# Optimization experiments

Measured on AMD Instinct MI355X. Metric: run time of the kernel, lower is better.

## Reference

```python
import jax, jax.numpy as jnp
import numpy as np

D_MODEL = 1024
NUM_HEADS = 16
D_HEAD = D_MODEL // NUM_HEADS
ROPE_THETA = 10000.0


def _rope(x, pos):
    # x: [..., S, d_head]; rotate consecutive pairs (2i, 2i+1)
    half = x.shape[-1] // 2
    inv_freq = ROPE_THETA ** (-jnp.arange(half, dtype=jnp.float32) * 2.0 / x.shape[-1])
    ang = pos[:, None].astype(jnp.float32) * inv_freq[None, :]  # [S, half]
    cos, sin = jnp.cos(ang), jnp.sin(ang)
    x1, x2 = x[..., 0::2], x[..., 1::2]
    r1 = x1 * cos - x2 * sin
    r2 = x1 * sin + x2 * cos
    return jnp.stack([r1, r2], axis=-1).reshape(x.shape)


def setup_inputs() -> dict:
    key = jax.random.key(0)
    ks = jax.random.split(key, 5)
    s = 1.0 / np.sqrt(D_MODEL)
    return {
        "q_weight": jax.random.normal(ks[0], (D_MODEL, D_MODEL), jnp.float32) * s,
        "k_weight": jax.random.normal(ks[1], (D_MODEL, D_MODEL), jnp.float32) * s,
        "v_weight": jax.random.normal(ks[2], (D_MODEL, D_MODEL), jnp.float32) * s,
        "o_weight": jax.random.normal(ks[3], (D_MODEL, D_MODEL), jnp.float32) * s,
        "in_features": jax.random.normal(ks[4], (2, 2048, D_MODEL), jnp.float32),
    }


def reference(q_weight, k_weight, v_weight, o_weight, in_features):
    S = in_features.shape[-2]
    qw = q_weight.reshape(NUM_HEADS, D_HEAD, D_MODEL)
    kw = k_weight.reshape(NUM_HEADS, D_HEAD, D_MODEL)
    vw = v_weight.reshape(NUM_HEADS, D_HEAD, D_MODEL)
    # [B, H, S, d_head]
    q = jnp.einsum('bsj,nhj->bnsh', in_features, qw)
    k = jnp.einsum('bsj,nhj->bnsh', in_features, kw)
    v = jnp.einsum('bsj,nhj->bnsh', in_features, vw)
    pos = jnp.arange(S)
    q = _rope(q, pos)
    k = _rope(k, pos)
    scale = 1.0 / jnp.sqrt(jnp.asarray(D_HEAD, dtype=q.dtype))
    scores = jnp.einsum('bnqh,bnkh->bnqk', q, k) * scale  # [B,H,S,S]
    causal = jnp.tril(jnp.ones((S, S), dtype=bool))
    scores = jnp.where(causal, scores, jnp.asarray(-jnp.inf, dtype=scores.dtype))
    attn = jax.nn.softmax(scores, axis=-1)
    out = jnp.einsum('bnqk,bnkh->bnqh', attn, v)  # [B,H,S,d_head]
    out = jnp.swapaxes(out, -2, -3).reshape(*out.shape[:-3], S, D_MODEL)
    return jnp.einsum('ji,bki->bkj', o_weight, out)
```

## Files before the change

### kernel.cpp

```cpp
#include <hip/hip_runtime.h>
#include <math.h>

typedef __attribute__((ext_vector_type(8))) short bf16x8;
typedef __attribute__((ext_vector_type(4))) short bf16x4;
typedef __attribute__((ext_vector_type(4))) float f32x4;
typedef __attribute__((ext_vector_type(2))) unsigned int u32x2;

static constexpr int D_MODEL = 1024;
static constexpr int SEQ = 2048;
static constexpr int BATCH = 2;
static constexpr int M_TOT = BATCH * SEQ;

__device__ __forceinline__ unsigned short f2bf(float f) {
  unsigned int u = __builtin_bit_cast(unsigned int, f);
  u += 0x7fffu + ((u >> 16) & 1u);
  return (unsigned short)(u >> 16);
}

__device__ __forceinline__ unsigned int cvtpk(float lo, float hi) {
  unsigned int r;
  asm volatile("v_cvt_pk_bf16_f32 %0, %1, %2" : "=v"(r) : "v"(lo), "v"(hi));
  return r;
}

__device__ __forceinline__ void gld16(const unsigned short* g, unsigned short* l) {
  __builtin_amdgcn_global_load_lds(
      (const __attribute__((address_space(1))) unsigned int*)g,
      (__attribute__((address_space(3))) unsigned int*)l, 16, 0, 0);
}

__global__ void prep_all(const float* __restrict__ x,
                         const float* __restrict__ qw, const float* __restrict__ kw,
                         const float* __restrict__ vw, const float* __restrict__ ow,
                         unsigned short* __restrict__ Xb,
                         unsigned short* __restrict__ Wqb,
                         float2* __restrict__ ct2) {
  constexpr int NX = M_TOT * D_MODEL / 4;
  constexpr int NW = D_MODEL * D_MODEL;
  const int i = blockIdx.x * blockDim.x + threadIdx.x;
  if (i < NX) {
    const float4 v = reinterpret_cast<const float4*>(x)[i];
    ushort4 o;
    o.x = f2bf(v.x); o.y = f2bf(v.y); o.z = f2bf(v.z); o.w = f2bf(v.w);
    reinterpret_cast<ushort4*>(Xb)[i] = o;
  } else if (i < NX + NW) {
    const int k = i - NX;
    const int which = k >> 18;
    const int off = k & 262143;
    const float* src = (which == 0) ? qw : (which == 1) ? kw : (which == 2) ? vw : ow;
    const float4 v = reinterpret_cast<const float4*>(src)[off];
    ushort4 o;
    o.x = f2bf(v.x); o.y = f2bf(v.y); o.z = f2bf(v.z); o.w = f2bf(v.w);
    reinterpret_cast<ushort4*>(Wqb)[k] = o;
  } else {
    const int k = i - NX - NW;
    const int s = k >> 5;
    const int p = k & 31;
    const float inv_freq = powf(10000.0f, -(float)p / 32.0f);
    const float ang = (float)s * inv_freq;
    const int psw = p ^ (((s >> 2) & 1) << 3);
    float2 cs; cs.x = cosf(ang); cs.y = sinf(ang);
    ct2[s * 32 + psw] = cs;
  }
}

template <int BM, int BN, int MODE>
__global__ __launch_bounds__(256, 2)
void gemm2(const unsigned short* __restrict__ A,
           const unsigned short* __restrict__ W,
           unsigned short* __restrict__ Qd,
           unsigned short* __restrict__ Kd,
           unsigned short* __restrict__ Vd,
           float* __restrict__ Fd,
           const float2* __restrict__ ct2) {
  constexpr int MI = BM / 32, NI = BN / 32;
  constexpr int NKT = D_MODEL / 64;
  constexpr int LOADS = BM / 32 + BN / 32;
  __shared__ __align__(16) unsigned short smem[2 * (BM + BN) * 64];
  unsigned short* Asm = smem;
  unsigned short* Bsm = smem + 2 * BM * 64;
  const int tid  = threadIdx.x;
  const int lane = tid & 63;
  const int wave = tid >> 6;
  const int wm = wave >> 1, wn = wave & 1;
  const int m0 = blockIdx.y * BM;
  const int n0 = blockIdx.x * BN;
  const int lr = lane & 15, lg = lane >> 4;

  auto stage = [&](int buf, int kt) {
    const int k0 = kt * 64;
#pragma unroll
    for (int c = 0; c < BM / 32; ++c) {
      const int ch = c * 4 + wave;
      const int row = ch * 8 + (lane >> 3);
      gld16(&A[(size_t)(m0 + row) * D_MODEL + k0 + ((lane & 7) ^ (row & 7)) * 8],
            &Asm[buf * BM * 64 + ch * 512]);
    }
#pragma unroll
    for (int c = 0; c < BN / 32; ++c) {
      const int ch = c * 4 + wave;
      const int row = ch * 8 + (lane >> 3);
      gld16(&W[(size_t)(n0 + row) * D_MODEL + k0 + ((lane & 7) ^ (row & 7)) * 8],
            &Bsm[buf * BN * 64 + ch * 512]);
    }
  };

  f32x4 acc[MI][NI] = {};

  stage(0, 0);
  stage(1, 1);
  __builtin_amdgcn_sched_barrier(0);

  for (int kt = 0; kt < NKT; ++kt) {
    const int cur = kt & 1;
    if (kt + 1 < NKT) {
      if constexpr (LOADS == 8) asm volatile("s_waitcnt vmcnt(8)" ::: "memory");
      else                      asm volatile("s_waitcnt vmcnt(6)" ::: "memory");
    } else {
      asm volatile("s_waitcnt vmcnt(0)" ::: "memory");
    }
    __builtin_amdgcn_s_barrier();
    __builtin_amdgcn_sched_barrier(0);

    bf16x8 af[MI][2], bfr[NI][2];
#pragma unroll
    for (int i = 0; i < MI; ++i)
#pragma unroll
      for (int ks = 0; ks < 2; ++ks) {
        const int R = wm * (BM / 2) + i * 16 + lr;
        const int p = (ks * 4 + lg) ^ (R & 7);
        af[i][ks] = *reinterpret_cast<const bf16x8*>(&Asm[cur * BM * 64 + R * 64 + p * 8]);
      }
#pragma unroll
    for (int j = 0; j < NI; ++j)
#pragma unroll
      for (int ks = 0; ks < 2; ++ks) {
        const int R = wn * (BN / 2) + j * 16 + lr;
        const int p = (ks * 4 + lg) ^ (R & 7);
        bfr[j][ks] = *reinterpret_cast<const bf16x8*>(&Bsm[cur * BN * 64 + R * 64 + p * 8]);
      }
    asm volatile("s_waitcnt lgkmcnt(0)" ::: "memory");
    __builtin_amdgcn_sched_barrier(0);
    __builtin_amdgcn_s_barrier();
    __builtin_amdgcn_sched_barrier(0);

    if (kt + 2 < NKT) stage(cur, kt + 2);
    __builtin_amdgcn_sched_barrier(0);

#pragma unroll
    for (int ks = 0; ks < 2; ++ks)
#pragma unroll
      for (int i = 0; i < MI; ++i)
#pragma unroll
        for (int j = 0; j < NI; ++j)
          acc[i][j] = __builtin_amdgcn_mfma_f32_16x16x32_bf16(af[i][ks], bfr[j][ks], acc[i][j], 0, 0, 0);
  }

  if constexpr (MODE == 2) {
#pragma unroll
    for (int i = 0; i < MI; ++i)
#pragma unroll
      for (int j = 0; j < NI; ++j)
#pragma unroll
        for (int r = 0; r < 4; ++r) {
          const int gm = m0 + wm * (BM / 2) + i * 16 + lg * 4 + r;
          const int gc = n0 + wn * (BN / 2) + j * 16 + lr;
          Fd[(size_t)gm * D_MODEL + gc] = acc[i][j][r];
        }
  } else {
    const int t = n0 >> 10;
    const int b = m0 >> 11;
    const int s_base = m0 & 2047;
    if (t < 2) {
      unsigned short* dstQ = (t == 0) ? Qd : Kd;
      const unsigned short* gsrc = (const unsigned short*)(ct2 + (size_t)s_base * 32);
#pragma unroll
      for (int it = 0; it < 8; ++it) {
        const int ch = wave * 8 + it;
        gld16(&gsrc[ch * 512 + lane * 8], &smem[ch * 512]);
      }
      asm volatile("s_waitcnt vmcnt(0)" ::: "memory");
      __builtin_amdgcn_sched_barrier(0);
      __builtin_amdgcn_s_barrier();
      const float2* tbl = (const float2*)smem;
      const int nbase = (n0 & 1023) >> 6;
#pragma unroll
      for (int i = 0; i < MI; ++i) {
#pragma unroll
        for (int j = 0; j < NI; ++j) {
#pragma unroll
          for (int r = 0; r < 4; ++r) {
            const int sl = wm * (BM / 2) + i * 16 + lg * 4 + r;
            const int h  = j * 16 + lr;
            const int psw = (h >> 1) ^ (((sl >> 2) & 1) << 3);
            const float2 cs = tbl[sl * 32 + psw];
            float x = acc[i][j][r];
            const float part = __shfl_xor(x, 1, 64);
            x = (h & 1) ? (part * cs.y + x * cs.x) : (x * cs.x - part * cs.y);
            const int n = nbase + wn;
            dstQ[(size_t)((b * 16 + n) * SEQ + s_base + sl) * 64 + h] = f2bf(x);
          }
        }
      }
    } else {
      unsigned short* tile = smem;
      const int row = tid >> 2;
      const int ck  = tid & 3;
      for (int pass = 0; pass < 2; ++pass) {
        __builtin_amdgcn_s_barrier();
        if (wn == pass) {
#pragma unroll
          for (int i = 0; i < MI; ++i)
#pragma unroll
            for (int j = 0; j < NI; ++j)
#pragma unroll
              for (int r = 0; r < 4; ++r)
                tile[(j * 16 + lr) * 136 + wm * 64 + i * 16 + lg * 4 + r] = f2bf(acc[i][j][r]);
        }
        asm volatile("s_waitcnt lgkmcnt(0)" ::: "memory");
        __builtin_amdgcn_sched_barrier(0);
        __builtin_amdgcn_s_barrier();
        const int c = (n0 & 1023) + pass * 64 + row;
        const int n = c >> 6, h = c & 63;
        unsigned short* vrow = &Vd[(size_t)((b * 16 + n) * 64 + h) * SEQ + s_base + ck * 32];
        const unsigned short* lrow = &tile[row * 136 + ck * 32];
#pragma unroll
        for (int k = 0; k < 4; ++k)
          *reinterpret_cast<bf16x8*>(&vrow[k * 8]) = *reinterpret_cast<const bf16x8*>(&lrow[k * 8]);
      }
    }
  }
}

__global__ __launch_bounds__(128, 2)
void attn_kernel(const unsigned short* __restrict__ Q,
                 const unsigned short* __restrict__ K,
                 const unsigned short* __restrict__ Vt,
                 unsigned short* __restrict__ AO) {
  __shared__ __align__(16) unsigned short Ksh[2][4096];
  __shared__ __align__(16) unsigned short Vsh[2][4096];
  const int bn   = blockIdx.x;
  const int y    = blockIdx.y;
  const int a    = y & 7, bsel = y >> 3;
  const int j    = (bsel == 0) ? (31 - a) : (bsel == 1) ? (16 + a)
                 : (bsel == 2) ? (15 - a) : a;
  const int wave = threadIdx.x >> 6;
  const int lane = threadIdx.x & 63;
  const int lr = lane & 15, lg = lane >> 4;
  const int q0 = j * 64 + wave * 32;
  const unsigned short* Qh = Q  + (size_t)bn * SEQ * 64;
  const unsigned short* Kh = K  + (size_t)bn * SEQ * 64;
  const unsigned short* Vh = Vt + (size_t)bn * 64 * SEQ;
  const int b = bn >> 4, n = bn & 15;

  const int srow8 = lane >> 3;
  const int scolb = ((lane & 7) ^ srow8) * 8;

  auto stage = [&](int buf, int k0) {
#pragma unroll
    for (int c = 0; c < 4; ++c) {
      const int ch = wave * 4 + c;
      const int row = ch * 8 + srow8;
      gld16(&Kh[(size_t)(k0 + row) * 64 + scolb], &Ksh[buf][ch * 512]);
      gld16(&Vh[(size_t)row * SEQ + k0 + scolb], &Vsh[buf][ch * 512]);
    }
  };

  constexpr float KL2E = 0.125f * 1.44269504088896f;
  const int nt = j + 1;

  bf16x8 qf[2][2];
#pragma unroll
  for (int mi = 0; mi < 2; ++mi)
#pragma unroll
    for (int ks = 0; ks < 2; ++ks)
      qf[mi][ks] = *reinterpret_cast<const bf16x8*>(
          &Qh[(size_t)(q0 + mi * 16 + lr) * 64 + ks * 32 + lg * 8]);
  asm volatile("s_waitcnt vmcnt(0)" ::: "memory");
  __builtin_amdgcn_sched_barrier(0);

  f32x4 o[2][4] = {};
  float ls[2] = {0.f, 0.f};

  stage(0, 0);
  stage(1, 64);
  __builtin_amdgcn_sched_barrier(0);

  for (int t = 0; t < nt; ++t) {
    const int cur = t & 1;
    const int k0 = t * 64;
    if (t + 1 < nt) { asm volatile("s_waitcnt vmcnt(8)" ::: "memory"); }
    else            { asm volatile("s_waitcnt vmcnt(0)" ::: "memory"); }
    __builtin_amdgcn_s_barrier();
    __builtin_amdgcn_sched_barrier(0);

    const unsigned short* Kc = &Ksh[cur][0];
    const unsigned short* Vc = &Vsh[cur][0];

    bf16x8 kf[4][2];
#pragma unroll
    for (int nj = 0; nj < 4; ++nj)
#pragma unroll
      for (int ks = 0; ks < 2; ++ks) {
        const int R = nj * 16 + lr;
        const int p = (ks * 4 + lg) ^ (R & 7);
        kf[nj][ks] = *reinterpret_cast<const bf16x8*>(&Kc[R * 64 + p * 8]);
      }
    f32x4 sf[2][4] = {};
    __builtin_amdgcn_s_setprio(1);
#pragma unroll
    for (int nj = 0; nj < 4; ++nj)
#pragma unroll
      for (int ks = 0; ks < 2; ++ks)
#pragma unroll
        for (int mi = 0; mi < 2; ++mi)
          sf[mi][nj] = __builtin_amdgcn_mfma_f32_16x16x32_bf16(kf[nj][ks], qf[mi][ks], sf[mi][nj], 0, 0, 0);
    __builtin_amdgcn_s_setprio(0);

    bf16x4 vB[4][4];
#pragma unroll
    for (int nj = 0; nj < 4; ++nj)
#pragma unroll
      for (int hf = 0; hf < 4; ++hf) {
        const int R = hf * 16 + lr;
        const int c = nj * 2 + (lg >> 1);
        const int p = ((c ^ (R & 7)) << 3) + (lg & 1) * 4;
        vB[nj][hf] = *reinterpret_cast<const bf16x4*>(&Vc[R * 64 + p]);
      }

    u32x2 w[2][4];
    if (k0 + 63 <= q0) {
#pragma unroll
      for (int mi = 0; mi < 2; ++mi)
#pragma unroll
        for (int nj = 0; nj < 4; ++nj) {
          const float p0 = __builtin_amdgcn_exp2f(sf[mi][nj][0] * KL2E);
          const float p1 = __builtin_amdgcn_exp2f(sf[mi][nj][1] * KL2E);
          const float p2 = __builtin_amdgcn_exp2f(sf[mi][nj][2] * KL2E);
          const float p3 = __builtin_amdgcn_exp2f(sf[mi][nj][3] * KL2E);
          ls[mi] += (p0 + p1) + (p2 + p3);
          w[mi][nj][0] = cvtpk(p0, p1);
          w[mi][nj][1] = cvtpk(p2, p3);
        }
    } else {
#pragma unroll
      for (int mi = 0; mi < 2; ++mi) {
        const int qrow = q0 + mi * 16 + lr;
#pragma unroll
        for (int nj = 0; nj < 4; ++nj) {
          const int kb = k0 + nj * 16 + lg * 4;
          float p[4];
#pragma unroll
          for (int r = 0; r < 4; ++r)
            p[r] = (kb + r <= qrow) ? __builtin_amdgcn_exp2f(sf[mi][nj][r] * KL2E) : 0.0f;
          ls[mi] += (p[0] + p[1]) + (p[2] + p[3]);
          w[mi][nj][0] = cvtpk(p[0], p[1]);
          w[mi][nj][1] = cvtpk(p[2], p[3]);
        }
      }
    }

    asm volatile("s_waitcnt lgkmcnt(0)" ::: "memory");
    __builtin_amdgcn_sched_barrier(0);
    __builtin_amdgcn_s_barrier();
    __builtin_amdgcn_sched_barrier(0);

    if (t + 2 < nt) stage(cur, (t + 2) * 64);
    __builtin_amdgcn_sched_barrier(0);

    __builtin_amdgcn_s_setprio(1);
#pragma unroll
    for (int nj = 0; nj < 4; ++nj)
#pragma unroll
      for (int hf = 0; hf < 4; ++hf)
#pragma unroll
        for (int mi = 0; mi < 2; ++mi)
          o[mi][hf] = __builtin_amdgcn_mfma_f32_16x16x16bf16_1k(
              __builtin_bit_cast(bf16x4, w[mi][nj]), vB[nj][hf], o[mi][hf], 0, 0, 0);
    __builtin_amdgcn_s_setprio(0);
  }

#pragma unroll
  for (int mi = 0; mi < 2; ++mi) {
    float s = ls[mi];
    s += __shfl_xor(s, 16, 64);
    s += __shfl_xor(s, 32, 64);
    ls[mi] = s;
  }
#pragma unroll
  for (int mi = 0; mi < 2; ++mi)
#pragma unroll
    for (int r = 0; r < 4; ++r) {
      const float sv = __shfl(ls[mi], lg * 4 + r, 64);
      const float inv = 1.0f / sv;
      const int srow = q0 + mi * 16 + lg * 4 + r;
#pragma unroll
      for (int hf = 0; hf < 4; ++hf) {
        const int h = hf * 16 + lr;
        AO[(size_t)(b * SEQ + srow) * D_MODEL + n * 64 + h] = f2bf(o[mi][hf][r] * inv);
      }
    }
}

extern "C" void kernel_launch(void* const* d_in, const int* in_sizes, int n_in,
                              void* d_out, int out_size, void* d_ws, size_t ws_size,
                              hipStream_t stream) {
  const float* qw = (const float*)d_in[0];
  const float* kw = (const float*)d_in[1];
  const float* vw = (const float*)d_in[2];
  const float* ow = (const float*)d_in[3];
  const float* x  = (const float*)d_in[4];

  char* ws = (char*)d_ws;
  const size_t XB = (size_t)M_TOT * D_MODEL * 2;
  const size_t WB = (size_t)D_MODEL * D_MODEL * 2;
  unsigned short* Xb  = (unsigned short*)ws;  ws += XB;
  unsigned short* Wqb = (unsigned short*)ws;  ws += WB;
  unsigned short* Wkb = (unsigned short*)ws;  ws += WB;
  unsigned short* Wvb = (unsigned short*)ws;  ws += WB;
  unsigned short* Wob = (unsigned short*)ws;  ws += WB;
  unsigned short* Qr  = (unsigned short*)ws;  ws += XB;
  unsigned short* Kr  = (unsigned short*)ws;  ws += XB;
  unsigned short* Vt  = (unsigned short*)ws;  ws += XB;
  unsigned short* AO  = (unsigned short*)ws;  ws += XB;
  float2* ct2 = (float2*)ws;  ws += (size_t)SEQ * 32 * 8;
  (void)Wkb; (void)Wvb;

  constexpr int PREP_ITEMS = M_TOT * D_MODEL / 4 + D_MODEL * D_MODEL + SEQ * 32;
  prep_all<<<(PREP_ITEMS + 255) / 256, 256, 0, stream>>>(x, qw, kw, vw, ow, Xb, Wqb, ct2);

  gemm2<128, 128, 0><<<dim3(3072 / 128, M_TOT / 128), 256, 0, stream>>>(
      Xb, Wqb, Qr, Kr, Vt, nullptr, ct2);

  attn_kernel<<<dim3(BATCH * 16, 32), 128, 0, stream>>>(Qr, Kr, Vt, AO);

  gemm2<128, 64, 2><<<dim3(D_MODEL / 64, M_TOT / 128), 256, 0, stream>>>(
      AO, Wob, nullptr, nullptr, nullptr, (float*)d_out, nullptr);
}
```

Measured before the change: 103.8 us.

## Enlarge attention query tiles and split long causal rows across two blocks

The attention kernel now uses 256 threads per block covering 128 query rows, so each K/V tile staged in shared memory is reused by four waves instead of two. For the eight longest query tiles, the key range is split into two halves handled by separate blocks. Each half writes unnormalized partial outputs and row sums into reused workspace buffers, and a new merge kernel adds the halves and normalizes. The intent is to balance causal work across blocks and improve K/V reuse. The cost is an extra kernel launch, bf16 rounding of the partial outputs, and extra global traffic.

```diff
diff --git a/kernel.cpp b/kernel.cpp
--- a/kernel.cpp
+++ b/kernel.cpp
@@ -15,6 +15,10 @@
   unsigned int u = __builtin_bit_cast(unsigned int, f);
   u += 0x7fffu + ((u >> 16) & 1u);
   return (unsigned short)(u >> 16);
+}
+
+__device__ __forceinline__ float bf2f(unsigned short u) {
+  return __builtin_bit_cast(float, (unsigned int)u << 16);
 }
 
 __device__ __forceinline__ unsigned int cvtpk(float lo, float hi) {
@@ -232,22 +236,26 @@
   }
 }
 
-__global__ __launch_bounds__(128, 2)
+__global__ __launch_bounds__(256, 2)
 void attn_kernel(const unsigned short* __restrict__ Q,
                  const unsigned short* __restrict__ K,
                  const unsigned short* __restrict__ Vt,
-                 unsigned short* __restrict__ AO) {
+                 unsigned short* __restrict__ AO,
+                 unsigned short* __restrict__ po,
+                 float* __restrict__ pl) {
   __shared__ __align__(16) unsigned short Ksh[2][4096];
   __shared__ __align__(16) unsigned short Vsh[2][4096];
   const int bn   = blockIdx.x;
   const int y    = blockIdx.y;
-  const int a    = y & 7, bsel = y >> 3;
-  const int j    = (bsel == 0) ? (31 - a) : (bsel == 1) ? (16 + a)
-                 : (bsel == 2) ? (15 - a) : a;
+  const bool split = (y < 16);
+  const int j    = split ? (15 - (y >> 1)) : (23 - y);
+  const int half = split ? (y & 1) : 0;
+  const int t0   = (split && half) ? (j + 1) : 0;
+  const int tend = (split && !half) ? (j + 1) : (2 * j + 2);
   const int wave = threadIdx.x >> 6;
   const int lane = threadIdx.x & 63;
   const int lr = lane & 15, lg = lane >> 4;
-  const int q0 = j * 64 + wave * 32;
+  const int q0 = j * 128 + wave * 32;
   const unsigned short* Qh = Q  + (size_t)bn * SEQ * 64;
   const unsigned short* Kh = K  + (size_t)bn * SEQ * 64;
   const unsigned short* Vh = Vt + (size_t)bn * 64 * SEQ;
@@ -258,8 +266,8 @@
 
   auto stage = [&](int buf, int k0) {
 #pragma unroll
-    for (int c = 0; c < 4; ++c) {
-      const int ch = wave * 4 + c;
+    for (int c = 0; c < 2; ++c) {
+      const int ch = wave * 2 + c;
       const int row = ch * 8 + srow8;
       gld16(&Kh[(size_t)(k0 + row) * 64 + scolb], &Ksh[buf][ch * 512]);
       gld16(&Vh[(size_t)row * SEQ + k0 + scolb], &Vsh[buf][ch * 512]);
@@ -267,7 +275,6 @@
   };
 
   constexpr float KL2E = 0.125f * 1.44269504088896f;
-  const int nt = j + 1;
 
   bf16x8 qf[2][2];
 #pragma unroll
@@ -282,15 +289,15 @@
   f32x4 o[2][4] = {};
   float ls[2] = {0.f, 0.f};
 
-  stage(0, 0);
-  stage(1, 64);
+  stage(0, t0 * 64);
+  stage(1, (t0 + 1) * 64);
   __builtin_amdgcn_sched_barrier(0);
 
-  for (int t = 0; t < nt; ++t) {
-    const int cur = t & 1;
+  for (int t = t0; t < tend; ++t) {
+    const int cur = (t - t0) & 1;
     const int k0 = t * 64;
-    if (t + 1 < nt) { asm volatile("s_waitcnt vmcnt(8)" ::: "memory"); }
-    else            { asm volatile("s_waitcnt vmcnt(0)" ::: "memory"); }
+    if (t + 1 < tend) { asm volatile("s_waitcnt vmcnt(4)" ::: "memory"); }
+    else              { asm volatile("s_waitcnt vmcnt(0)" ::: "memory"); }
     __builtin_amdgcn_s_barrier();
     __builtin_amdgcn_sched_barrier(0);
 
@@ -365,7 +372,7 @@
     __builtin_amdgcn_s_barrier();
     __builtin_amdgcn_sched_barrier(0);
 
-    if (t + 2 < nt) stage(cur, (t + 2) * 64);
+    if (t + 2 < tend) stage(cur, (t + 2) * 64);
     __builtin_amdgcn_sched_barrier(0);
 
     __builtin_amdgcn_s_setprio(1);
@@ -387,19 +394,62 @@
     s += __shfl_xor(s, 32, 64);
     ls[mi] = s;
   }
-#pragma unroll
-  for (int mi = 0; mi < 2; ++mi)
-#pragma unroll
-    for (int r = 0; r < 4; ++r) {
-      const float sv = __shfl(ls[mi], lg * 4 + r, 64);
-      const float inv = 1.0f / sv;
-      const int srow = q0 + mi * 16 + lg * 4 + r;
-#pragma unroll
-      for (int hf = 0; hf < 4; ++hf) {
-        const int h = hf * 16 + lr;
-        AO[(size_t)(b * SEQ + srow) * D_MODEL + n * 64 + h] = f2bf(o[mi][hf][r] * inv);
-      }
-    }
+
+  if (!split) {
+#pragma unroll
+    for (int mi = 0; mi < 2; ++mi)
+#pragma unroll
+      for (int r = 0; r < 4; ++r) {
+        const float sv = __shfl(ls[mi], lg * 4 + r, 64);
+        const float inv = 1.0f / sv;
+        const int srow = q0 + mi * 16 + lg * 4 + r;
+#pragma unroll
+        for (int hf = 0; hf < 4; ++hf) {
+          const int h = hf * 16 + lr;
+          AO[(size_t)(b * SEQ + srow) * D_MODEL + n * 64 + h] = f2bf(o[mi][hf][r] * inv);
+        }
+      }
+  } else {
+    const int pb = (bn * 8 + (j - 8)) * 2 + half;
+    unsigned short* pod = po + (size_t)pb * (128 * 64);
+    float* pld = pl + (size_t)pb * 128;
+    if (lg == 0) {
+#pragma unroll
+      for (int mi = 0; mi < 2; ++mi)
+        pld[wave * 32 + mi * 16 + lr] = ls[mi];
+    }
+#pragma unroll
+    for (int mi = 0; mi < 2; ++mi)
+#pragma unroll
+      for (int r = 0; r < 4; ++r) {
+        const int row = wave * 32 + mi * 16 + lg * 4 + r;
+#pragma unroll
+        for (int hf = 0; hf < 4; ++hf)
+          pod[row * 64 + hf * 16 + lr] = f2bf(o[mi][hf][r]);
+      }
+  }
+}
+
+__global__ void attn_merge(const unsigned short* __restrict__ po,
+                           const float* __restrict__ pl,
+                           unsigned short* __restrict__ AO) {
+  const int i = blockIdx.x * blockDim.x + threadIdx.x;
+  const int g   = i & 7;
+  const int row = (i >> 3) & 127;
+  const int jj  = (i >> 10) & 7;
+  const int bn  = i >> 13;
+  const int pb0 = (bn * 8 + jj) * 2;
+  const float l = pl[pb0 * 128 + row] + pl[(pb0 + 1) * 128 + row];
+  const float inv = 1.0f / l;
+  const bf16x8 a = *reinterpret_cast<const bf16x8*>(&po[(size_t)pb0 * 8192 + row * 64 + g * 8]);
+  const bf16x8 c = *reinterpret_cast<const bf16x8*>(&po[(size_t)(pb0 + 1) * 8192 + row * 64 + g * 8]);
+  bf16x8 out;
+#pragma unroll
+  for (int e = 0; e < 8; ++e)
+    out[e] = (short)f2bf((bf2f((unsigned short)a[e]) + bf2f((unsigned short)c[e])) * inv);
+  const int s = (jj + 8) * 128 + row;
+  const int b = bn >> 4, n = bn & 15;
+  *reinterpret_cast<bf16x8*>(&AO[(size_t)(b * SEQ + s) * D_MODEL + n * 64 + g * 8]) = out;
 }
 
 extern "C" void kernel_launch(void* const* d_in, const int* in_sizes, int n_in,
@@ -426,13 +476,18 @@
   float2* ct2 = (float2*)ws;  ws += (size_t)SEQ * 32 * 8;
   (void)Wkb; (void)Wvb;
 
+  unsigned short* po = Xb;
+  float*          pl = (float*)Wqb;
+
   constexpr int PREP_ITEMS = M_TOT * D_MODEL / 4 + D_MODEL * D_MODEL + SEQ * 32;
   prep_all<<<(PREP_ITEMS + 255) / 256, 256, 0, stream>>>(x, qw, kw, vw, ow, Xb, Wqb, ct2);
 
   gemm2<128, 128, 0><<<dim3(3072 / 128, M_TOT / 128), 256, 0, stream>>>(
       Xb, Wqb, Qr, Kr, Vt, nullptr, ct2);
 
-  attn_kernel<<<dim3(BATCH * 16, 32), 128, 0, stream>>>(Qr, Kr, Vt, AO);
+  attn_kernel<<<dim3(BATCH * 16, 24), 256, 0, stream>>>(Qr, Kr, Vt, AO, po, pl);
+
+  attn_merge<<<262144 / 256, 256, 0, stream>>>(po, pl, AO);
 
   gemm2<128, 64, 2><<<dim3(D_MODEL / 64, M_TOT / 128), 256, 0, stream>>>(
       AO, Wob, nullptr, nullptr, nullptr, (float*)d_out, nullptr);
```

Result: no change. 102.8 us (-1.0%).
